# Kernel tuning notes

Hardware: AMD Instinct MI355X
Metric: run time of the kernel (lower is better)

Reference implementation:

```python
import jax, jax.numpy as jnp
import numpy as np

B, T, V, S_FIXED, DIM, CV = 4, 256, 1024, 64, 1024, 256


def setup_inputs() -> dict:
    key = jax.random.key(0)
    ks = jax.random.split(key, 8)
    x = jax.random.normal(ks[0], (B, T, DIM), jnp.float32)
    vision = jax.random.normal(ks[1], (B, V, CV), jnp.float32)
    # attention mask (B, V, T): each text token t attends to exactly S_FIXED vision tokens
    scores = jax.random.uniform(ks[2], (B, T, V))
    _, sel = jax.lax.top_k(scores, S_FIXED)  # (B, T, S)
    mask_tv = jnp.zeros((B, T, V), bool)
    mask_tv = mask_tv.at[jnp.arange(B)[:, None, None], jnp.arange(T)[None, :, None], sel].set(True)
    attention_mask = jnp.transpose(mask_tv, (0, 2, 1))  # (B, V, T)
    # xavier-uniform-like params (scale irrelevant for correctness baseline)
    Wu = jax.random.normal(ks[3], (CV, DIM), jnp.float32) * (1.0 / np.sqrt(CV))
    bu = jax.random.normal(ks[4], (DIM,), jnp.float32) * 0.02
    Wk = jax.random.normal(ks[5], (DIM, DIM), jnp.float32) * (1.0 / np.sqrt(DIM))
    Wv = jax.random.normal(ks[6], (DIM, DIM), jnp.float32) * (1.0 / np.sqrt(DIM))
    return {"x": x, "vision": vision, "attention_mask": attention_mask,
            "Wu": Wu, "bu": bu, "Wk": Wk, "Wv": Wv, "S": S_FIXED}


def reference(x, vision, attention_mask, Wu, bu, Wk, Wv, S):
    Bv, Vn, Cv = vision.shape
    Bx, Tn, C = x.shape  # C == dim
    # --- _construct_sparse_inputs ---
    mask_tv = jnp.transpose(attention_mask, (0, 2, 1))  # (B, T, V)
    idx_full = jnp.where(mask_tv, jnp.arange(Vn, dtype=jnp.int32), jnp.int32(Vn))
    # topk(largest=False) == smallest S indices, ascending; pad value = Vn
    index = -jax.lax.top_k(-idx_full, S)[0]  # (B, T, S)
    vision_pad = jnp.concatenate([vision, jnp.zeros((Bv, 1, Cv), vision.dtype)], axis=1)  # (B, V+1, Cv)
    vg = jnp.take_along_axis(vision_pad, index.reshape(Bv, Tn * S, 1), axis=1)
    vg = vg.reshape(Bv, Tn, S, Cv)  # (B, T, S, 256)
    # NOTE: faithful to source — VALID positions receive the -100 bias
    mask_qk = (index != Vn)[..., None].astype(jnp.float32) * (-100.0)  # (B, T, S, 1)
    # --- attention ---
    vu = vg @ Wu + bu           # (B, T, S, dim)
    k = vu @ Wk                 # (B, T, S, dim)
    v = vu @ Wv                 # (B, T, S, dim)
    q = x[:, :, None, :]        # (B, T, 1, dim)
    qk = jnp.einsum('bksc,bktc->bkst', k, q) / jnp.sqrt(jnp.float32(C)) + mask_qk  # (B, T, S, 1)
    sm = jax.nn.softmax(qk.reshape(Bx, -1), axis=-1).reshape(qk.shape)  # softmax over flattened T*S*1
    attn = jnp.einsum('bkst,bksc->bktc', sm, v)  # (B, T, 1, dim)
    return (attn + q).squeeze(2)  # (B, T, dim)
```

## Files before the change

kernel.cpp:

```cpp
#include <hip/hip_runtime.h>
#include <stdint.h>

#define B 4
#define T 256
#define V 1024
#define S 64
#define DIM 1024
#define CV 256

typedef __attribute__((ext_vector_type(8))) short bf16x8;
typedef __attribute__((ext_vector_type(4))) short s16x4;
typedef __attribute__((ext_vector_type(4))) float f32x4;

enum : int {
    WKT_O   = 0,
    WVT_O   = WKT_O + 262144,
    WUB_O   = WVT_O + 262144,
    WKPB_O  = WUB_O + 131072,
    WVPT_O  = WKPB_O + 131072,
    XB_O    = WVPT_O + 131072,
    ZB_O    = XB_O + 262144,
    VB_O    = ZB_O + 131072,
    WB_O    = VB_O + 524288,
    RS_O    = WB_O + 131072,
    PIDX_O  = RS_O + B*T,
    BK_O    = PIDX_O + B*T*S,
    BV_O    = BK_O + DIM,
    BP_O    = BV_O + DIM,
    WS_TOTAL= BP_O + 2*16*1024
};

__device__ __forceinline__ short f2bf(float f) {
    union { float f; unsigned u; } x; x.f = f;
    unsigned r = (x.u + 0x7FFF + ((x.u >> 16) & 1)) >> 16;
    return (short)r;
}
__device__ __forceinline__ float bf2f(short s) {
    union { unsigned u; float f; } x;
    x.u = ((unsigned)(unsigned short)s) << 16;
    return x.f;
}
__device__ __forceinline__ s16x4 cvt4(float4 f) {
    s16x4 o;
    o.x = f2bf(f.x); o.y = f2bf(f.y); o.z = f2bf(f.z); o.w = f2bf(f.w);
    return o;
}

__global__ void stage1(const float* __restrict__ vision, const float* __restrict__ Wu,
                       const float* __restrict__ x, const float* __restrict__ Wk,
                       const float* __restrict__ Wv, const float* __restrict__ bu,
                       const void* __restrict__ maskp,
                       float* __restrict__ ws, int* __restrict__ wsi) {
    __shared__ short tlds[64 * 65];
    __shared__ float tred[4 * 64];
    __shared__ int mc_cnt[16][17];
    __shared__ int sa_flag, sb_flag;
    int blk = blockIdx.x;
    int tid = threadIdx.x;

    if (blk < 2304) {
        const float* src; short* dst; int idx;
        if (blk < 1024)      { src = vision; dst = (short*)(ws + VB_O);  idx = blk; }
        else if (blk < 1280) { src = Wu;     dst = (short*)(ws + WUB_O); idx = blk - 1024; }
        else                 { src = x;      dst = (short*)(ws + XB_O);  idx = blk - 1280; }
        int i = (idx * 256 + tid);
        ((s16x4*)dst)[i] = cvt4(((const float4*)src)[i]);
        return;
    }
    if (blk < 2816) {
        int tile = blk - 2304;
        int which = tile >> 8, t2 = tile & 255;
        int e0 = (t2 >> 4) * 64, d0 = (t2 & 15) * 64;
        const float* src = which ? Wv : Wk;
        short* dst = (short*)(ws + (which ? WVT_O : WKT_O));
        int j = tid & 63, i0 = tid >> 6;
        float pb = 0.f;
#pragma unroll
        for (int p = 0; p < 16; p++) {
            int i = p * 4 + i0;
            float v = src[(size_t)(e0 + i) * DIM + d0 + j];
            tlds[j * 65 + i] = f2bf(v);
            pb += bu[e0 + i] * v;
        }
        tred[i0 * 64 + j] = pb;
        __syncthreads();
#pragma unroll
        for (int p = 0; p < 16; p++) {
            int dd = p * 4 + i0;
            dst[(size_t)(d0 + dd) * DIM + e0 + j] = tlds[dd * 65 + j];
        }
        if (i0 == 0) {
            float s = tred[j] + tred[64 + j] + tred[128 + j] + tred[192 + j];
            ws[BP_O + (which * 16 + (e0 >> 6)) * 1024 + d0 + j] = s;
        }
        return;
    }
    {
        int a = 0, bfl = 0;
        const uchar4* m4 = (const uchar4*)maskp;
#pragma unroll
        for (int jj = 0; jj < 4; jj++) {
            uchar4 u = m4[tid * 4 + jj];
            if (u.y | u.z | u.w) a = 1;
            if (u.x == 0x3f || u.y == 0x3f || u.z == 0x3f || u.w == 0x3f) bfl = 1;
        }
        if (tid == 0) { sa_flag = 0; sb_flag = 0; }
        __syncthreads();
        if (a) sa_flag = 1;
        if (bfl) sb_flag = 1;
        __syncthreads();
    }
    bool byteMode = sa_flag && !sb_flag;
    int mb = blk - 2816;
    int b = mb >> 4, tg = mb & 15;
    int tl = tid & 15, c = tid >> 4;
    int t = tg * 16 + tl;
    int v0 = c * 64;
    unsigned long long bits = 0ull;
    if (byteMode) {
        const uint8_t* m = (const uint8_t*)maskp + (size_t)(b * V + v0) * T + t;
#pragma unroll 8
        for (int j = 0; j < 64; j++)
            if (m[(size_t)j * T] != 0) bits |= 1ull << j;
    } else {
        const int* m = (const int*)maskp + (size_t)(b * V + v0) * T + t;
#pragma unroll 8
        for (int j = 0; j < 64; j++)
            if (m[(size_t)j * T] != 0) bits |= 1ull << j;
    }
    mc_cnt[tl][c] = __popcll(bits);
    __syncthreads();
    int off = 0, total = 0;
#pragma unroll
    for (int cc = 0; cc < 16; cc++) {
        int cn = mc_cnt[tl][cc];
        if (cc < c) off += cn;
        total += cn;
    }
    int base = PIDX_O + (b * T + t) * S;
    while (bits) {
        int j = __ffsll(bits) - 1;
        bits &= bits - 1;
        if (off < S) wsi[base + off] = v0 + j;
        off++;
    }
    if (c == 15)
        for (int j = (total < S ? total : S); j < S; j++) wsi[base + j] = 0;
}

template<int K, int LDA, int LDB>
__device__ __forceinline__ void wave_mma(const short* __restrict__ A0,
                                         const short* __restrict__ B0,
                                         f32x4 acc[2][2]) {
    int lane = threadIdx.x & 63;
    int rw = lane & 15, q = lane >> 4;
    const short* ap0 = A0 + rw * LDA + q * 8;
    const short* ap1 = ap0 + 16 * LDA;
    const short* bp0 = B0 + rw * LDB + q * 8;
    const short* bp1 = bp0 + 16 * LDB;
#pragma unroll 4
    for (int kc = 0; kc < K; kc += 32) {
        bf16x8 a0 = *(const bf16x8*)(ap0 + kc);
        bf16x8 a1 = *(const bf16x8*)(ap1 + kc);
        bf16x8 b0 = *(const bf16x8*)(bp0 + kc);
        bf16x8 b1 = *(const bf16x8*)(bp1 + kc);
        acc[0][0] = __builtin_amdgcn_mfma_f32_16x16x32_bf16(a0, b0, acc[0][0], 0, 0, 0);
        acc[0][1] = __builtin_amdgcn_mfma_f32_16x16x32_bf16(a0, b1, acc[0][1], 0, 0, 0);
        acc[1][0] = __builtin_amdgcn_mfma_f32_16x16x32_bf16(a1, b0, acc[1][0], 0, 0, 0);
        acc[1][1] = __builtin_amdgcn_mfma_f32_16x16x32_bf16(a1, b1, acc[1][1], 0, 0, 0);
    }
}

__device__ __forceinline__ bool splitk_reduce(f32x4 acc[2][2],
                                              float (*red)[64][17],
                                              int wv, int lane) {
    if (wv > 0) {
#pragma unroll
        for (int i = 0; i < 2; i++)
#pragma unroll
            for (int j = 0; j < 2; j++)
#pragma unroll
                for (int r = 0; r < 4; r++)
                    red[wv - 1][lane][(i * 2 + j) * 4 + r] = acc[i][j][r];
    }
    __syncthreads();
    if (wv != 0) return false;
#pragma unroll
    for (int i = 0; i < 2; i++)
#pragma unroll
        for (int j = 0; j < 2; j++)
#pragma unroll
            for (int r = 0; r < 4; r++) {
                int c = (i * 2 + j) * 4 + r;
                acc[i][j][r] += red[0][lane][c] + red[1][lane][c] + red[2][lane][c];
            }
    return true;
}

__global__ void g_prep_mfma(float* __restrict__ ws) {
    if (blockIdx.x >= 512) {
        int which = blockIdx.x - 512;
#pragma unroll
        for (int cch = 0; cch < 4; cch++) {
            int d = cch * 256 + threadIdx.x;
            float s = 0.f;
#pragma unroll
            for (int g = 0; g < 16; g++)
                s += ws[BP_O + (which * 16 + g) * 1024 + d];
            ws[(which ? BV_O : BK_O) + d] = s;
        }
        return;
    }
    __shared__ float red[3][64][17];
    int tile = blockIdx.x;
    int which = tile >> 8, rem = tile & 255;
    int m0 = (rem >> 5) * 32, n0 = (rem & 31) * 32;
    int wv = threadIdx.x >> 6, lane = threadIdx.x & 63;
    const short* A = (const short*)(ws + WUB_O) + (size_t)m0 * DIM + wv * 256;
    const short* Bt = (const short*)(ws + (which ? WVT_O : WKT_O)) + (size_t)n0 * DIM + wv * 256;
    f32x4 acc[2][2] = {};
    wave_mma<256, DIM, DIM>(A, Bt, acc);
    if (!splitk_reduce(acc, red, wv, lane)) return;
    int col = lane & 15, q = lane >> 4;
    if (which == 0) {
        short* o = (short*)(ws + WKPB_O);
#pragma unroll
        for (int i = 0; i < 2; i++)
#pragma unroll
            for (int j = 0; j < 2; j++)
#pragma unroll
                for (int r = 0; r < 4; r++)
                    o[(size_t)(m0 + i * 16 + q * 4 + r) * DIM + n0 + j * 16 + col] =
                        f2bf(acc[i][j][r]);
    } else {
        short* o = (short*)(ws + WVPT_O);
#pragma unroll
        for (int i = 0; i < 2; i++)
#pragma unroll
            for (int j = 0; j < 2; j++) {
                s16x4 v;
                v.x = f2bf(acc[i][j][0]); v.y = f2bf(acc[i][j][1]);
                v.z = f2bf(acc[i][j][2]); v.w = f2bf(acc[i][j][3]);
                *(s16x4*)&o[(size_t)(n0 + j * 16 + col) * CV + m0 + i * 16 + q * 4] = v;
            }
    }
}

__global__ void g_z_mfma(float* __restrict__ ws) {
    __shared__ float red[3][64][17];
    int w = blockIdx.x;
    int m0 = (w >> 3) * 32, n0 = (w & 7) * 32;
    int wv = threadIdx.x >> 6, lane = threadIdx.x & 63;
    const short* A = (const short*)(ws + XB_O) + (size_t)m0 * DIM + wv * 256;
    const short* Bt = (const short*)(ws + WKPB_O) + (size_t)n0 * DIM + wv * 256;
    f32x4 acc[2][2] = {};
    wave_mma<256, DIM, DIM>(A, Bt, acc);
    if (!splitk_reduce(acc, red, wv, lane)) return;
    int col = lane & 15, q = lane >> 4;
    short* zb = (short*)(ws + ZB_O);
#pragma unroll
    for (int i = 0; i < 2; i++)
#pragma unroll
        for (int j = 0; j < 2; j++)
#pragma unroll
            for (int r = 0; r < 4; r++)
                zb[(size_t)(m0 + i * 16 + q * 4 + r) * CV + n0 + j * 16 + col] =
                    f2bf(acc[i][j][r]);
}

__global__ void g_attn(const float* __restrict__ x, float* __restrict__ ws,
                       int* __restrict__ wsi) {
    __shared__ int   s_idx[2][64];
    __shared__ float s_sc[2][64];
    __shared__ float s_c0[2][2];
    __shared__ float s_p[2][64];
    __shared__ float s_wa[2][64][5];
    int tid = threadIdx.x;
    int lane = tid & 63, wv = tid >> 6;
    int pair = wv >> 1, h = wv & 1;
    int bt = blockIdx.x * 2 + pair, b = bt >> 8;
    if (h == 0) s_idx[pair][lane] = wsi[PIDX_O + bt * S + lane];
    float c0p = 0.f;
    const float4* xr = (const float4*)(x + (size_t)bt * DIM);
    const float4* bkr = (const float4*)(ws + BK_O);
#pragma unroll
    for (int j = 0; j < 2; j++) {
        int jj = h * 2 + j;
        float4 a = xr[lane + 64 * jj], k4 = bkr[lane + 64 * jj];
        c0p += a.x * k4.x + a.y * k4.y + a.z * k4.z + a.w * k4.w;
    }
    for (int o = 32; o > 0; o >>= 1) c0p += __shfl_xor(c0p, o);
    if (lane == 0) s_c0[pair][h] = c0p;
    __syncthreads();
    int rw = lane & 15, q = lane >> 4;
    const short* vb = (const short*)(ws + VB_O) + (size_t)b * V * CV;
    const short* zp = (const short*)(ws + ZB_O) + (size_t)bt * CV + q * 8;
#pragma unroll
    for (int mi = 0; mi < 2; mi++) {
        int mt = h * 2 + mi;
        const short* ap = vb + (size_t)s_idx[pair][mt * 16 + rw] * CV + q * 8;
        f32x4 a4 = {0.f, 0.f, 0.f, 0.f};
#pragma unroll
        for (int kc = 0; kc < CV; kc += 32) {
            bf16x8 av = *(const bf16x8*)(ap + kc);
            bf16x8 bv = *(const bf16x8*)(zp + kc);
            a4 = __builtin_amdgcn_mfma_f32_16x16x32_bf16(av, bv, a4, 0, 0, 0);
        }
        if (rw == 0) {
#pragma unroll
            for (int r = 0; r < 4; r++)
                s_sc[pair][mt * 16 + q * 4 + r] = a4[r];
        }
    }
    __syncthreads();
    float c0 = s_c0[pair][0] + s_c0[pair][1];
    float p = expf((s_sc[pair][lane] + c0) * 0.03125f);
    float rs = p;
    for (int o = 32; o > 0; o >>= 1) rs += __shfl_xor(rs, o);
    s_p[pair][lane] = p;
    if (h == 0 && lane == 0) ws[RS_O + bt] = rs;
    float4 wa = {0.f, 0.f, 0.f, 0.f};
#pragma unroll 8
    for (int si = 0; si < 32; si++) {
        int s = h * 32 + si;
        float pv = s_p[pair][s];
        s16x4 r4 = *(const s16x4*)(vb + (size_t)s_idx[pair][s] * CV + lane * 4);
        wa.x += pv * bf2f(r4.x); wa.y += pv * bf2f(r4.y);
        wa.z += pv * bf2f(r4.z); wa.w += pv * bf2f(r4.w);
    }
    if (h == 1) {
        s_wa[pair][lane][0] = wa.x; s_wa[pair][lane][1] = wa.y;
        s_wa[pair][lane][2] = wa.z; s_wa[pair][lane][3] = wa.w;
    }
    __syncthreads();
    if (h == 0) {
        wa.x += s_wa[pair][lane][0]; wa.y += s_wa[pair][lane][1];
        wa.z += s_wa[pair][lane][2]; wa.w += s_wa[pair][lane][3];
        s16x4 o;
        o.x = f2bf(wa.x); o.y = f2bf(wa.y); o.z = f2bf(wa.z); o.w = f2bf(wa.w);
        ((s16x4*)((short*)(ws + WB_O) + (size_t)bt * CV))[lane] = o;
    }
}

__global__ void g_out_mfma(const float* __restrict__ x, float* __restrict__ ws,
                           float* __restrict__ out) {
    int w = blockIdx.x * 4 + (threadIdx.x >> 6);
    int m0 = (w >> 6) * 32, n0 = (w & 63) * 16;
    int lane = threadIdx.x & 63;
    int b = m0 >> 8;
    float4 r4 = *(const float4*)(ws + RS_O + b * 256 + lane * 4);
    float dn = r4.x + r4.y + r4.z + r4.w;
    for (int o = 32; o > 0; o >>= 1) dn += __shfl_xor(dn, o);
    float inv = 1.0f / dn;
    int rw = lane & 15, q = lane >> 4;
    const short* A  = (const short*)(ws + WB_O)   + (size_t)m0 * CV;
    const short* Bt = (const short*)(ws + WVPT_O) + (size_t)n0 * CV;
    const short* ap0 = A + rw * CV + q * 8;
    const short* ap1 = ap0 + 16 * CV;
    const short* bp0 = Bt + rw * CV + q * 8;
    f32x4 acc[2] = {};
#pragma unroll 4
    for (int kc = 0; kc < CV; kc += 32) {
        bf16x8 a0 = *(const bf16x8*)(ap0 + kc);
        bf16x8 a1 = *(const bf16x8*)(ap1 + kc);
        bf16x8 b0 = *(const bf16x8*)(bp0 + kc);
        acc[0] = __builtin_amdgcn_mfma_f32_16x16x32_bf16(a0, b0, acc[0], 0, 0, 0);
        acc[1] = __builtin_amdgcn_mfma_f32_16x16x32_bf16(a1, b0, acc[1], 0, 0, 0);
    }
    int col = lane & 15;
#pragma unroll
    for (int i = 0; i < 2; i++)
#pragma unroll
        for (int r = 0; r < 4; r++) {
            int row = m0 + i * 16 + q * 4 + r;
            float rs = ws[RS_O + row];
            int cc = n0 + col;
            out[(size_t)row * DIM + cc] =
                x[(size_t)row * DIM + cc] +
                (acc[i][r] + rs * ws[BV_O + cc]) * inv;
        }
}

extern "C" void kernel_launch(void* const* d_in, const int* in_sizes, int n_in,
                              void* d_out, int out_size, void* d_ws, size_t ws_size,
                              hipStream_t stream) {
    (void)in_sizes; (void)n_in; (void)out_size; (void)ws_size;
    const float* x      = (const float*)d_in[0];
    const float* vision = (const float*)d_in[1];
    const void*  mask   = d_in[2];
    const float* Wu     = (const float*)d_in[3];
    const float* bu     = (const float*)d_in[4];
    const float* Wk     = (const float*)d_in[5];
    const float* Wv     = (const float*)d_in[6];
    float* out = (float*)d_out;
    float* ws  = (float*)d_ws;
    int*   wsi = (int*)d_ws;

    stage1<<<2880, 256, 0, stream>>>(vision, Wu, x, Wk, Wv, bu, mask, ws, wsi);
    g_prep_mfma<<<514, 256, 0, stream>>>(ws);
    g_z_mfma<<<256, 256, 0, stream>>>(ws);
    g_attn<<<512, 256, 0, stream>>>(x, ws, wsi);
    g_out_mfma<<<512, 256, 0, stream>>>(x, ws, out);
}
```

Before: 115.7 us.

## Fuse five kernel launches into one cooperative persistent kernel with grid syncs

Measured after the change: 363.1 us. 214% more time.

```diff
diff --git a/kernel.cpp b/kernel.cpp
--- a/kernel.cpp
+++ b/kernel.cpp
@@ -1,5 +1,8 @@
 #include <hip/hip_runtime.h>
+#include <hip/hip_cooperative_groups.h>
 #include <stdint.h>
+
+namespace cg = cooperative_groups;
 
 #define B 4
 #define T 256
@@ -46,28 +49,32 @@
     return o;
 }
 
-__global__ void stage1(const float* __restrict__ vision, const float* __restrict__ Wu,
-                       const float* __restrict__ x, const float* __restrict__ Wk,
-                       const float* __restrict__ Wv, const float* __restrict__ bu,
-                       const void* __restrict__ maskp,
-                       float* __restrict__ ws, int* __restrict__ wsi) {
-    __shared__ short tlds[64 * 65];
-    __shared__ float tred[4 * 64];
-    __shared__ int mc_cnt[16][17];
-    __shared__ int sa_flag, sb_flag;
-    int blk = blockIdx.x;
-    int tid = threadIdx.x;
-
+struct SMem {
+    union U {
+        struct S1 { short tlds[64 * 65]; float tred[256]; int mc[16][17]; int saf, sbf; } s1;
+        float red[3][64][17];
+        struct AT { int idx[2][64]; float sc[2][64]; float c0q[2][2]; float p[2][64]; float wa[2][64][5]; } at;
+    } u;
+};
+
+__device__ __forceinline__ void phase_s1(int blk, int tid,
+        const float* __restrict__ vision, const float* __restrict__ Wu,
+        const float* __restrict__ x, const float* __restrict__ Wk,
+        const float* __restrict__ Wv, const float* __restrict__ bu,
+        const void* __restrict__ maskp, float* __restrict__ ws,
+        int* __restrict__ wsi, SMem* sm) {
     if (blk < 2304) {
         const float* src; short* dst; int idx;
         if (blk < 1024)      { src = vision; dst = (short*)(ws + VB_O);  idx = blk; }
         else if (blk < 1280) { src = Wu;     dst = (short*)(ws + WUB_O); idx = blk - 1024; }
         else                 { src = x;      dst = (short*)(ws + XB_O);  idx = blk - 1280; }
-        int i = (idx * 256 + tid);
+        int i = idx * 256 + tid;
         ((s16x4*)dst)[i] = cvt4(((const float4*)src)[i]);
         return;
     }
     if (blk < 2816) {
+        short* tlds = sm->u.s1.tlds;
+        float* tred = sm->u.s1.tred;
         int tile = blk - 2304;
         int which = tile >> 8, t2 = tile & 255;
         int e0 = (t2 >> 4) * 64, d0 = (t2 & 15) * 64;
@@ -104,13 +111,13 @@
             if (u.y | u.z | u.w) a = 1;
             if (u.x == 0x3f || u.y == 0x3f || u.z == 0x3f || u.w == 0x3f) bfl = 1;
         }
-        if (tid == 0) { sa_flag = 0; sb_flag = 0; }
+        if (tid == 0) { sm->u.s1.saf = 0; sm->u.s1.sbf = 0; }
         __syncthreads();
-        if (a) sa_flag = 1;
-        if (bfl) sb_flag = 1;
+        if (a) sm->u.s1.saf = 1;
+        if (bfl) sm->u.s1.sbf = 1;
         __syncthreads();
     }
-    bool byteMode = sa_flag && !sb_flag;
+    bool byteMode = sm->u.s1.saf && !sm->u.s1.sbf;
     int mb = blk - 2816;
     int b = mb >> 4, tg = mb & 15;
     int tl = tid & 15, c = tid >> 4;
@@ -128,12 +135,12 @@
         for (int j = 0; j < 64; j++)
             if (m[(size_t)j * T] != 0) bits |= 1ull << j;
     }
-    mc_cnt[tl][c] = __popcll(bits);
+    sm->u.s1.mc[tl][c] = __popcll(bits);
     __syncthreads();
     int off = 0, total = 0;
 #pragma unroll
     for (int cc = 0; cc < 16; cc++) {
-        int cn = mc_cnt[tl][cc];
+        int cn = sm->u.s1.mc[tl][cc];
         if (cc < c) off += cn;
         total += cn;
     }
@@ -197,12 +204,14 @@
     return true;
 }
 
-__global__ void g_prep_mfma(float* __restrict__ ws) {
-    if (blockIdx.x >= 512) {
-        int which = blockIdx.x - 512;
+__device__ __forceinline__ void phase_prep(int blk, int tid, float* __restrict__ ws,
+                                           SMem* sm) {
+    if (blk >= 514) return;
+    if (blk >= 512) {
+        int which = blk - 512;
 #pragma unroll
         for (int cch = 0; cch < 4; cch++) {
-            int d = cch * 256 + threadIdx.x;
+            int d = cch * 256 + tid;
             float s = 0.f;
 #pragma unroll
             for (int g = 0; g < 16; g++)
@@ -211,16 +220,14 @@
         }
         return;
     }
-    __shared__ float red[3][64][17];
-    int tile = blockIdx.x;
-    int which = tile >> 8, rem = tile & 255;
+    int which = blk >> 8, rem = blk & 255;
     int m0 = (rem >> 5) * 32, n0 = (rem & 31) * 32;
-    int wv = threadIdx.x >> 6, lane = threadIdx.x & 63;
+    int wv = tid >> 6, lane = tid & 63;
     const short* A = (const short*)(ws + WUB_O) + (size_t)m0 * DIM + wv * 256;
     const short* Bt = (const short*)(ws + (which ? WVT_O : WKT_O)) + (size_t)n0 * DIM + wv * 256;
     f32x4 acc[2][2] = {};
     wave_mma<256, DIM, DIM>(A, Bt, acc);
-    if (!splitk_reduce(acc, red, wv, lane)) return;
+    if (!splitk_reduce(acc, sm->u.red, wv, lane)) return;
     int col = lane & 15, q = lane >> 4;
     if (which == 0) {
         short* o = (short*)(ws + WKPB_O);
@@ -246,16 +253,15 @@
     }
 }
 
-__global__ void g_z_mfma(float* __restrict__ ws) {
-    __shared__ float red[3][64][17];
-    int w = blockIdx.x;
-    int m0 = (w >> 3) * 32, n0 = (w & 7) * 32;
-    int wv = threadIdx.x >> 6, lane = threadIdx.x & 63;
+__device__ __forceinline__ void phase_z(int blk, int tid, float* __restrict__ ws,
+                                        SMem* sm) {
+    int m0 = (blk >> 3) * 32, n0 = (blk & 7) * 32;
+    int wv = tid >> 6, lane = tid & 63;
     const short* A = (const short*)(ws + XB_O) + (size_t)m0 * DIM + wv * 256;
     const short* Bt = (const short*)(ws + WKPB_O) + (size_t)n0 * DIM + wv * 256;
     f32x4 acc[2][2] = {};
     wave_mma<256, DIM, DIM>(A, Bt, acc);
-    if (!splitk_reduce(acc, red, wv, lane)) return;
+    if (!splitk_reduce(acc, sm->u.red, wv, lane)) return;
     int col = lane & 15, q = lane >> 4;
     short* zb = (short*)(ws + ZB_O);
 #pragma unroll
@@ -268,18 +274,13 @@
                     f2bf(acc[i][j][r]);
 }
 
-__global__ void g_attn(const float* __restrict__ x, float* __restrict__ ws,
-                       int* __restrict__ wsi) {
-    __shared__ int   s_idx[2][64];
-    __shared__ float s_sc[2][64];
-    __shared__ float s_c0[2][2];
-    __shared__ float s_p[2][64];
-    __shared__ float s_wa[2][64][5];
-    int tid = threadIdx.x;
+__device__ __forceinline__ void phase_attn(int blk, int tid, const float* __restrict__ x,
+                                           float* __restrict__ ws, int* __restrict__ wsi,
+                                           SMem* sm) {
     int lane = tid & 63, wv = tid >> 6;
     int pair = wv >> 1, h = wv & 1;
-    int bt = blockIdx.x * 2 + pair, b = bt >> 8;
-    if (h == 0) s_idx[pair][lane] = wsi[PIDX_O + bt * S + lane];
+    int bt = blk * 2 + pair, b = bt >> 8;
+    if (h == 0) sm->u.at.idx[pair][lane] = wsi[PIDX_O + bt * S + lane];
     float c0p = 0.f;
     const float4* xr = (const float4*)(x + (size_t)bt * DIM);
     const float4* bkr = (const float4*)(ws + BK_O);
@@ -290,7 +291,7 @@
         c0p += a.x * k4.x + a.y * k4.y + a.z * k4.z + a.w * k4.w;
     }
     for (int o = 32; o > 0; o >>= 1) c0p += __shfl_xor(c0p, o);
-    if (lane == 0) s_c0[pair][h] = c0p;
+    if (lane == 0) sm->u.at.c0q[pair][h] = c0p;
     __syncthreads();
     int rw = lane & 15, q = lane >> 4;
     const short* vb = (const short*)(ws + VB_O) + (size_t)b * V * CV;
@@ -298,7 +299,7 @@
 #pragma unroll
     for (int mi = 0; mi < 2; mi++) {
         int mt = h * 2 + mi;
-        const short* ap = vb + (size_t)s_idx[pair][mt * 16 + rw] * CV + q * 8;
+        const short* ap = vb + (size_t)sm->u.at.idx[pair][mt * 16 + rw] * CV + q * 8;
         f32x4 a4 = {0.f, 0.f, 0.f, 0.f};
 #pragma unroll
         for (int kc = 0; kc < CV; kc += 32) {
@@ -309,44 +310,44 @@
         if (rw == 0) {
 #pragma unroll
             for (int r = 0; r < 4; r++)
-                s_sc[pair][mt * 16 + q * 4 + r] = a4[r];
+                sm->u.at.sc[pair][mt * 16 + q * 4 + r] = a4[r];
         }
     }
     __syncthreads();
-    float c0 = s_c0[pair][0] + s_c0[pair][1];
-    float p = expf((s_sc[pair][lane] + c0) * 0.03125f);
+    float c0 = sm->u.at.c0q[pair][0] + sm->u.at.c0q[pair][1];
+    float p = expf((sm->u.at.sc[pair][lane] + c0) * 0.03125f);
     float rs = p;
     for (int o = 32; o > 0; o >>= 1) rs += __shfl_xor(rs, o);
-    s_p[pair][lane] = p;
+    sm->u.at.p[pair][lane] = p;
     if (h == 0 && lane == 0) ws[RS_O + bt] = rs;
     float4 wa = {0.f, 0.f, 0.f, 0.f};
 #pragma unroll 8
     for (int si = 0; si < 32; si++) {
         int s = h * 32 + si;
-        float pv = s_p[pair][s];
-        s16x4 r4 = *(const s16x4*)(vb + (size_t)s_idx[pair][s] * CV + lane * 4);
+        float pv = sm->u.at.p[pair][s];
+        s16x4 r4 = *(const s16x4*)(vb + (size_t)sm->u.at.idx[pair][s] * CV + lane * 4);
         wa.x += pv * bf2f(r4.x); wa.y += pv * bf2f(r4.y);
         wa.z += pv * bf2f(r4.z); wa.w += pv * bf2f(r4.w);
     }
     if (h == 1) {
-        s_wa[pair][lane][0] = wa.x; s_wa[pair][lane][1] = wa.y;
-        s_wa[pair][lane][2] = wa.z; s_wa[pair][lane][3] = wa.w;
+        sm->u.at.wa[pair][lane][0] = wa.x; sm->u.at.wa[pair][lane][1] = wa.y;
+        sm->u.at.wa[pair][lane][2] = wa.z; sm->u.at.wa[pair][lane][3] = wa.w;
     }
     __syncthreads();
     if (h == 0) {
-        wa.x += s_wa[pair][lane][0]; wa.y += s_wa[pair][lane][1];
-        wa.z += s_wa[pair][lane][2]; wa.w += s_wa[pair][lane][3];
+        wa.x += sm->u.at.wa[pair][lane][0]; wa.y += sm->u.at.wa[pair][lane][1];
+        wa.z += sm->u.at.wa[pair][lane][2]; wa.w += sm->u.at.wa[pair][lane][3];
         s16x4 o;
         o.x = f2bf(wa.x); o.y = f2bf(wa.y); o.z = f2bf(wa.z); o.w = f2bf(wa.w);
         ((s16x4*)((short*)(ws + WB_O) + (size_t)bt * CV))[lane] = o;
     }
 }
 
-__global__ void g_out_mfma(const float* __restrict__ x, float* __restrict__ ws,
-                           float* __restrict__ out) {
-    int w = blockIdx.x * 4 + (threadIdx.x >> 6);
+__device__ __forceinline__ void phase_out(int blk, int tid, const float* __restrict__ x,
+                                          float* __restrict__ ws, float* __restrict__ out) {
+    int w = blk * 4 + (tid >> 6);
     int m0 = (w >> 6) * 32, n0 = (w & 63) * 16;
-    int lane = threadIdx.x & 63;
+    int lane = tid & 63;
     int b = m0 >> 8;
     float4 r4 = *(const float4*)(ws + RS_O + b * 256 + lane * 4);
     float dn = r4.x + r4.y + r4.z + r4.w;
@@ -381,6 +382,54 @@
         }
 }
 
+__global__ void __launch_bounds__(256, 2)
+mega(const float* __restrict__ vision, const float* __restrict__ Wu,
+     const float* __restrict__ x, const float* __restrict__ Wk,
+     const float* __restrict__ Wv, const float* __restrict__ bu,
+     const void* __restrict__ maskp, float* __restrict__ ws,
+     int* __restrict__ wsi, float* __restrict__ out) {
+    __shared__ SMem sm;
+    cg::grid_group g = cg::this_grid();
+    int tid = threadIdx.x, blk = blockIdx.x;
+    for (int u = blk; u < 2880; u += 512) {
+        phase_s1(u, tid, vision, Wu, x, Wk, Wv, bu, maskp, ws, wsi, &sm);
+        __syncthreads();
+    }
+    g.sync();
+    for (int u = blk; u < 514; u += 512) {
+        phase_prep(u, tid, ws, &sm);
+        __syncthreads();
+    }
+    g.sync();
+    if (blk < 256) phase_z(blk, tid, ws, &sm);
+    g.sync();
+    phase_attn(blk, tid, x, ws, wsi, &sm);
+    g.sync();
+    phase_out(blk, tid, x, ws, out);
+}
+
+__global__ void stage1_k(const float* vision, const float* Wu, const float* x,
+                         const float* Wk, const float* Wv, const float* bu,
+                         const void* maskp, float* ws, int* wsi) {
+    __shared__ SMem sm;
+    phase_s1(blockIdx.x, threadIdx.x, vision, Wu, x, Wk, Wv, bu, maskp, ws, wsi, &sm);
+}
+__global__ void g_prep_k(float* ws) {
+    __shared__ SMem sm;
+    phase_prep(blockIdx.x, threadIdx.x, ws, &sm);
+}
+__global__ void g_z_k(float* ws) {
+    __shared__ SMem sm;
+    phase_z(blockIdx.x, threadIdx.x, ws, &sm);
+}
+__global__ void g_attn_k(const float* x, float* ws, int* wsi) {
+    __shared__ SMem sm;
+    phase_attn(blockIdx.x, threadIdx.x, x, ws, wsi, &sm);
+}
+__global__ void g_out_k(const float* x, float* ws, float* out) {
+    phase_out(blockIdx.x, threadIdx.x, x, ws, out);
+}
+
 extern "C" void kernel_launch(void* const* d_in, const int* in_sizes, int n_in,
                               void* d_out, int out_size, void* d_ws, size_t ws_size,
                               hipStream_t stream) {
@@ -396,9 +445,15 @@
     float* ws  = (float*)d_ws;
     int*   wsi = (int*)d_ws;
 
-    stage1<<<2880, 256, 0, stream>>>(vision, Wu, x, Wk, Wv, bu, mask, ws, wsi);
-    g_prep_mfma<<<514, 256, 0, stream>>>(ws);
-    g_z_mfma<<<256, 256, 0, stream>>>(ws);
-    g_attn<<<512, 256, 0, stream>>>(x, ws, wsi);
-    g_out_mfma<<<512, 256, 0, stream>>>(x, ws, out);
-}
+    void* args[] = {(void*)&vision, (void*)&Wu, (void*)&x, (void*)&Wk, (void*)&Wv,
+                    (void*)&bu, (void*)&mask, (void*)&ws, (void*)&wsi, (void*)&out};
+    hipError_t e = hipLaunchCooperativeKernel((const void*)mega, dim3(512), dim3(256),
+                                              args, 0, stream);
+    if (e != hipSuccess) {
+        stage1_k<<<2880, 256, 0, stream>>>(vision, Wu, x, Wk, Wv, bu, mask, ws, wsi);
+        g_prep_k<<<514, 256, 0, stream>>>(ws);
+        g_z_k<<<256, 256, 0, stream>>>(ws);
+        g_attn_k<<<512, 256, 0, stream>>>(x, ws, wsi);
+        g_out_k<<<512, 256, 0, stream>>>(x, ws, out);
+    }
+}
```

## Stage gathered vision rows in swizzled LDS, one token per block

Applied to the files above, without the earlier changes.

After: 116.5 us. Within noise of the previous version (+0.6%).

```diff
diff --git a/kernel.cpp b/kernel.cpp
--- a/kernel.cpp
+++ b/kernel.cpp
@@ -268,74 +268,87 @@
                     f2bf(acc[i][j][r]);
 }
 
-__global__ void g_attn(const float* __restrict__ x, float* __restrict__ ws,
-                       int* __restrict__ wsi) {
-    __shared__ int   s_idx[2][64];
-    __shared__ float s_sc[2][64];
-    __shared__ float s_c0[2][2];
-    __shared__ float s_p[2][64];
-    __shared__ float s_wa[2][64][5];
+__global__ void __launch_bounds__(256, 4)
+g_attn(const float* __restrict__ x, float* __restrict__ ws,
+       int* __restrict__ wsi) {
+    __shared__ short svr[64 * 256];
+    __shared__ int   s_idx[64];
+    __shared__ float s_sc[64];
+    __shared__ float s_c0[4];
+    __shared__ float s_wa[3][64][5];
     int tid = threadIdx.x;
     int lane = tid & 63, wv = tid >> 6;
-    int pair = wv >> 1, h = wv & 1;
-    int bt = blockIdx.x * 2 + pair, b = bt >> 8;
-    if (h == 0) s_idx[pair][lane] = wsi[PIDX_O + bt * S + lane];
-    float c0p = 0.f;
-    const float4* xr = (const float4*)(x + (size_t)bt * DIM);
-    const float4* bkr = (const float4*)(ws + BK_O);
-#pragma unroll
-    for (int j = 0; j < 2; j++) {
-        int jj = h * 2 + j;
-        float4 a = xr[lane + 64 * jj], k4 = bkr[lane + 64 * jj];
-        c0p += a.x * k4.x + a.y * k4.y + a.z * k4.z + a.w * k4.w;
-    }
-    for (int o = 32; o > 0; o >>= 1) c0p += __shfl_xor(c0p, o);
-    if (lane == 0) s_c0[pair][h] = c0p;
+    int blk = blockIdx.x;
+    int bt = ((blk & 7) << 7) + (blk >> 3);
+    int b = bt >> 8;
+
+    if (tid < 64) s_idx[tid] = wsi[PIDX_O + bt * S + tid];
+    {
+        const float4* xr = (const float4*)(x + (size_t)bt * DIM);
+        const float4* bkr = (const float4*)(ws + BK_O);
+        float4 a = xr[wv * 64 + lane], k4 = bkr[wv * 64 + lane];
+        float c0p = a.x * k4.x + a.y * k4.y + a.z * k4.z + a.w * k4.w;
+        for (int o = 32; o > 0; o >>= 1) c0p += __shfl_xor(c0p, o);
+        if (lane == 0) s_c0[wv] = c0p;
+    }
+    __syncthreads();
+    const short* vb = (const short*)(ws + VB_O) + (size_t)b * V * CV;
+    {
+        int r = tid >> 2, part = tid & 3;
+        const bf16x8* src = (const bf16x8*)(vb + (size_t)s_idx[r] * CV);
+#pragma unroll
+        for (int i = 0; i < 8; i++) {
+            int c = part * 8 + i;
+            int sl = c ^ (r & 7);
+            *(bf16x8*)((char*)svr + r * 512 + sl * 16) = src[c];
+        }
+    }
     __syncthreads();
     int rw = lane & 15, q = lane >> 4;
-    const short* vb = (const short*)(ws + VB_O) + (size_t)b * V * CV;
-    const short* zp = (const short*)(ws + ZB_O) + (size_t)bt * CV + q * 8;
-#pragma unroll
-    for (int mi = 0; mi < 2; mi++) {
-        int mt = h * 2 + mi;
-        const short* ap = vb + (size_t)s_idx[pair][mt * 16 + rw] * CV + q * 8;
+    {
+        const short* zp = (const short*)(ws + ZB_O) + (size_t)bt * CV + q * 8;
+        int srow = wv * 16 + rw;
         f32x4 a4 = {0.f, 0.f, 0.f, 0.f};
 #pragma unroll
-        for (int kc = 0; kc < CV; kc += 32) {
-            bf16x8 av = *(const bf16x8*)(ap + kc);
-            bf16x8 bv = *(const bf16x8*)(zp + kc);
+        for (int kc8 = 0; kc8 < 8; kc8++) {
+            int sl = (q + kc8 * 4) ^ (srow & 7);
+            bf16x8 av = *(const bf16x8*)((char*)svr + srow * 512 + sl * 16);
+            bf16x8 bv = *(const bf16x8*)(zp + kc8 * 32);
             a4 = __builtin_amdgcn_mfma_f32_16x16x32_bf16(av, bv, a4, 0, 0, 0);
         }
         if (rw == 0) {
 #pragma unroll
             for (int r = 0; r < 4; r++)
-                s_sc[pair][mt * 16 + q * 4 + r] = a4[r];
-        }
-    }
-    __syncthreads();
-    float c0 = s_c0[pair][0] + s_c0[pair][1];
-    float p = expf((s_sc[pair][lane] + c0) * 0.03125f);
+                s_sc[wv * 16 + q * 4 + r] = a4[r];
+        }
+    }
+    __syncthreads();
+    float c0 = s_c0[0] + s_c0[1] + s_c0[2] + s_c0[3];
+    float p = expf((s_sc[lane] + c0) * 0.03125f);
     float rs = p;
     for (int o = 32; o > 0; o >>= 1) rs += __shfl_xor(rs, o);
-    s_p[pair][lane] = p;
-    if (h == 0 && lane == 0) ws[RS_O + bt] = rs;
+    if (tid == 0) ws[RS_O + bt] = rs;
     float4 wa = {0.f, 0.f, 0.f, 0.f};
-#pragma unroll 8
-    for (int si = 0; si < 32; si++) {
-        int s = h * 32 + si;
-        float pv = s_p[pair][s];
-        s16x4 r4 = *(const s16x4*)(vb + (size_t)s_idx[pair][s] * CV + lane * 4);
+#pragma unroll
+    for (int si = 0; si < 16; si++) {
+        int s = wv * 16 + si;
+        float pv = __shfl(p, s);
+        int sl = (lane >> 1) ^ (s & 7);
+        s16x4 r4 = *(const s16x4*)((char*)svr + s * 512 + sl * 16 + (lane & 1) * 8);
         wa.x += pv * bf2f(r4.x); wa.y += pv * bf2f(r4.y);
         wa.z += pv * bf2f(r4.z); wa.w += pv * bf2f(r4.w);
     }
-    if (h == 1) {
-        s_wa[pair][lane][0] = wa.x; s_wa[pair][lane][1] = wa.y;
-        s_wa[pair][lane][2] = wa.z; s_wa[pair][lane][3] = wa.w;
-    }
-    __syncthreads();
-    if (h == 0) {
-        wa.x += s_wa[pair][lane][0]; wa.y += s_wa[pair][lane][1];
-        wa.z += s_wa[pair][lane][2]; wa.w += s_wa[pair][lane][3];
+    if (wv > 0) {
+        s_wa[wv - 1][lane][0] = wa.x; s_wa[wv - 1][lane][1] = wa.y;
+        s_wa[wv - 1][lane][2] = wa.z; s_wa[wv - 1][lane][3] = wa.w;
+    }
+    __syncthreads();
+    if (wv == 0) {
+#pragma unroll
+        for (int g = 0; g < 3; g++) {
+            wa.x += s_wa[g][lane][0]; wa.y += s_wa[g][lane][1];
+            wa.z += s_wa[g][lane][2]; wa.w += s_wa[g][lane][3];
+        }
         s16x4 o;
         o.x = f2bf(wa.x); o.y = f2bf(wa.y); o.z = f2bf(wa.z); o.w = f2bf(wa.w);
         ((s16x4*)((short*)(ws + WB_O) + (size_t)bt * CV))[lane] = o;
@@ -399,6 +412,6 @@
     stage1<<<2880, 256, 0, stream>>>(vision, Wu, x, Wk, Wv, bu, mask, ws, wsi);
     g_prep_mfma<<<514, 256, 0, stream>>>(ws);
     g_z_mfma<<<256, 256, 0, stream>>>(ws);
-    g_attn<<<512, 256, 0, stream>>>(x, ws, wsi);
+    g_attn<<<1024, 256, 0, stream>>>(x, ws, wsi);
     g_out_mfma<<<512, 256, 0, stream>>>(x, ws, out);
 }
```
